# Kernel tuning notes

Hardware: AMD Instinct MI355X
Metric: run time of the kernel (lower is better)

## Reference

```python
import jax, jax.numpy as jnp
import numpy as np

B, P, Q, A, H = 8, 512, 64, 16, 128
H2, H10, G = 2 * H, 10 * H, 3 * H


def setup_inputs() -> dict:
    key = jax.random.key(0)
    ks = jax.random.split(key, 40)
    n = lambda k, s, sc=1.0: jax.random.normal(k, s, jnp.float32) * sc
    W = 0.05  # xavier-ish small init so tanh stays in linear-ish range
    inp = {
        "passage_enc": n(ks[0], (B, P, H2)),
        "query_enc": n(ks[1], (B, Q, H2)),
        "alt1_enc": n(ks[2], (B, A, H)),
        "alt2_enc": n(ks[3], (B, A, H)),
        "alt3_enc": n(ks[4], (B, A, H)),
        "a_att_w": n(ks[5], (H,), W),
        "Wc1": n(ks[6], (H2, H), W), "Wc2": n(ks[7], (H2, H), W), "vc": n(ks[8], (H,), W),
        "Wb": n(ks[9], (H2, H2), W),
        "Wd": n(ks[10], (H2, H), W), "vd": n(ks[11], (H,), W),
        "Wm": n(ks[12], (H2, H), W), "vm": n(ks[13], (H,), W),
        "wq": n(ks[14], (H2, H), W), "vq": n(ks[15], (H,), W),
        "wp1": n(ks[16], (H2, H), W), "wp2": n(ks[17], (H2, H), W), "vp": n(ks[18], (H,), W),
        "predict_w": n(ks[19], (H2, H), W),
        "gWih_f": n(ks[20], (H10, G), W), "gWhh_f": n(ks[21], (H, G), W),
        "gbih_f": jnp.zeros((G,), jnp.float32), "gbhh_f": jnp.zeros((G,), jnp.float32),
        "gWih_b": n(ks[22], (H10, G), W), "gWhh_b": n(ks[23], (H, G), W),
        "gbih_b": jnp.zeros((G,), jnp.float32), "gbhh_b": jnp.zeros((G,), jnp.float32),
        "passage_mask": jnp.ones((B, P), jnp.int32),
        "query_mask": jnp.ones((B, Q), jnp.int32),
        "alt1_mask": jnp.ones((B, A), jnp.int32),
        "alt2_mask": jnp.ones((B, A), jnp.int32),
        "alt3_mask": jnp.ones((B, A), jnp.int32),
    }
    return inp


def _att_pool(x, w, mask):
    # x: (B,T,D), w: (D,) -> (B,D) masked-softmax attention pooling
    s = jnp.where(mask != 0, x @ w, -jnp.inf)
    a = jax.nn.softmax(s, axis=1)
    return jnp.einsum('bt,btd->bd', a, x)


def _masked_attend(scores, qmask, query):
    # scores: (B,P,Q); mask over query axis, softmax over Q, weighted sum of query
    s = jnp.where(qmask[:, None, :] != 0, scores, -jnp.inf)
    a = jax.nn.softmax(s, axis=2)
    return jnp.einsum('bpq,bqd->bpd', a, query)


def _gru_dir(x, Wih, Whh, bih, bhh, reverse):
    # x: (B,T,Din) -> (B,T,H), PyTorch GRU gate convention
    if reverse:
        x = x[:, ::-1]
    gi = x @ Wih + bih  # (B,T,3H)
    h0 = jnp.zeros((x.shape[0], Whh.shape[0]), x.dtype)

    def step(h, gi_t):
        gh = h @ Whh + bhh
        i_r, i_z, i_n = jnp.split(gi_t, 3, axis=-1)
        h_r, h_z, h_n = jnp.split(gh, 3, axis=-1)
        r = jax.nn.sigmoid(i_r + h_r)
        z = jax.nn.sigmoid(i_z + h_z)
        nn_ = jnp.tanh(i_n + r * h_n)
        h_new = (1.0 - z) * nn_ + z * h
        return h_new, h_new

    _, ys = jax.lax.scan(step, h0, jnp.swapaxes(gi, 0, 1))
    ys = jnp.swapaxes(ys, 0, 1)
    if reverse:
        ys = ys[:, ::-1]
    return ys


def _forward(passage_enc, query_enc, alt1_enc, alt2_enc, alt3_enc,
             a_att_w, Wc1, Wc2, vc, Wb, Wd, vd, Wm, vm,
             wq, vq, wp1, wp2, vp, predict_w,
             gWih_f, gWhh_f, gbih_f, gbhh_f, gWih_b, gWhh_b, gbih_b, gbhh_b,
             passage_mask, query_mask, alt1_mask, alt2_mask, alt3_mask):
    # --- alternative-answer pooling ---
    a1 = _att_pool(alt1_enc, a_att_w, alt1_mask)
    a2 = _att_pool(alt2_enc, a_att_w, alt2_mask)
    a3 = _att_pool(alt3_enc, a_att_w, alt3_mask)

    # --- multi-hop passage-query attention (4 score variants) ---
    p1 = passage_enc @ Wc1          # (B,P,H)
    q1 = query_enc @ Wc2            # (B,Q,H)
    sc_c = jnp.einsum('bpqh,h->bpq', jnp.tanh(p1[:, :, None, :] + q1[:, None, :, :]), vc)
    pc = _masked_attend(sc_c, query_mask, query_enc)

    sc_b = jnp.einsum('bpd,bqd->bpq', passage_enc @ Wb, query_enc)
    pb = _masked_attend(sc_b, query_mask, query_enc)

    # Wd(p * q) with elementwise product, then tanh, then vd
    sc_d = jnp.einsum('bpqh,h->bpq',
                      jnp.tanh(jnp.einsum('bpk,bqk,kh->bpqh', passage_enc, query_enc, Wd)), vd)
    pd = _masked_attend(sc_d, query_mask, query_enc)

    # Wm(q - p) = q@Wm - p@Wm (linearity)
    pmq = query_enc @ Wm            # (B,Q,H)
    pmp = passage_enc @ Wm          # (B,P,H)
    sc_m = jnp.einsum('bpqh,h->bpq', jnp.tanh(pmq[:, None, :, :] - pmp[:, :, None, :]), vm)
    pm = _masked_attend(sc_m, query_mask, query_enc)

    # --- aggregation bi-GRU over (B,P,10H) ---
    agg_in = jnp.concatenate([passage_enc, pc, pb, pd, pm], axis=2)
    h_f = _gru_dir(agg_in, gWih_f, gWhh_f, gbih_f, gbhh_f, reverse=False)
    h_b = _gru_dir(agg_in, gWih_b, gWhh_b, gbih_b, gbhh_b, reverse=True)
    agg = jnp.concatenate([h_f, h_b], axis=2)   # (B,P,2H)

    # --- query summary rq ---
    sj = jnp.where(query_mask != 0, jnp.tanh(query_enc @ wq) @ vq, -jnp.inf)
    sj = jax.nn.softmax(sj, axis=1)
    rq = jnp.einsum('bq,bqd->bd', sj, query_enc)   # (B,2H)

    # --- passage summary rp attended by rq ---
    sp = jnp.tanh(agg @ wp1 + (rq @ wp2)[:, None, :]) @ vp   # (B,P)
    sp = jnp.where(passage_mask != 0, sp, -jnp.inf)
    sp = jax.nn.softmax(sp, axis=1)
    rp = jnp.einsum('bp,bpd->bd', sp, agg)          # (B,2H)
    rp = jax.nn.leaky_relu(rp @ predict_w)          # (B,H), slope 0.01

    alters = jnp.stack([a1, a2, a3], axis=1)        # (B,3,H)
    logits = jnp.einsum('bah,bh->ba', alters, rp)
    return jax.nn.softmax(logits, axis=1)


def reference(passage_enc, query_enc, alt1_enc, alt2_enc, alt3_enc,
              a_att_w, Wc1, Wc2, vc, Wb, Wd, vd, Wm, vm,
              wq, vq, wp1, wp2, vp, predict_w,
              gWih_f, gWhh_f, gbih_f, gbhh_f, gWih_b, gWhh_b, gbih_b, gbhh_b,
              passage_mask, query_mask, alt1_mask, alt2_mask, alt3_mask):
    return _forward(passage_enc, query_enc, alt1_enc, alt2_enc, alt3_enc,
                    a_att_w, Wc1, Wc2, vc, Wb, Wd, vd, Wm, vm,
                    wq, vq, wp1, wp2, vp, predict_w,
                    gWih_f, gWhh_f, gbih_f, gbhh_f, gWih_b, gWhh_b, gbih_b, gbhh_b,
                    passage_mask, query_mask, alt1_mask, alt2_mask, alt3_mask)
```

## Files before the change

### kernel.cpp

```cpp
#include <hip/hip_runtime.h>

#define B_ 8
#define P_ 512
#define Q_ 64
#define A_ 16
#define H_ 128
#define H2_ 256
#define H10_ 1280
#define G_ 384

typedef float f32x4 __attribute__((ext_vector_type(4)));
typedef _Float16 half4_t __attribute__((ext_vector_type(4)));
typedef _Float16 half8_t __attribute__((ext_vector_type(8)));

__device__ __forceinline__ float fast_tanh(float x) {
  return 1.f - 2.f * __builtin_amdgcn_rcpf(1.f + __builtin_amdgcn_exp2f(2.88539008f * x));
}
__device__ __forceinline__ float fast_sigm(float x) {
  return __builtin_amdgcn_rcpf(1.f + __builtin_amdgcn_exp2f(-1.44269504f * x));
}

#define GRUBAR() asm volatile("s_waitcnt lgkmcnt(0)\n\ts_barrier" ::: "memory")

#define NB_PRE 6936

__device__ __forceinline__ void prep_frag_body(int idx, const float* __restrict__ W,
                                               _Float16* __restrict__ out, int KT, int HT, int N) {
  int total = KT * HT * 64 * 4;
  if (idx >= total) return;
  int e = idx & 3;
  int l = (idx >> 2) & 63;
  int rest = idx >> 8;
  int ht = rest % HT;
  int ks = rest / HT;
  int k = ks * 16 + ((l >> 4) << 2) + e;
  int n = ht * 16 + (l & 15);
  out[idx] = (_Float16)W[(size_t)k * N + n];
}

__device__ __forceinline__ void prep_frag32_body(int idx, const float* __restrict__ W,
                                                 _Float16* __restrict__ out, int KT, int HT, int N) {
  int total = KT * HT * 64 * 8;
  if (idx >= total) return;
  int e = idx & 7;
  int l = (idx >> 3) & 63;
  int rest = idx >> 9;
  int ht = rest % HT;
  int ks = rest / HT;
  int k = ks * 32 + ((l >> 4) << 3) + e;
  int n = ht * 16 + (l & 15);
  out[idx] = (_Float16)W[(size_t)k * N + n];
}

__global__ __launch_bounds__(256) void k_pre(
    const float* __restrict__ a1, const float* __restrict__ a2, const float* __restrict__ a3,
    const int* __restrict__ m1, const int* __restrict__ m2, const int* __restrict__ m3,
    const float* __restrict__ a_att_w, float* __restrict__ alters,
    const float* __restrict__ Wd, _Float16* __restrict__ wd_sw,
    const float* __restrict__ gWih_f, const float* __restrict__ gWih_b,
    _Float16* __restrict__ gih_sw,
    const float* __restrict__ gWhh_f, const float* __restrict__ gWhh_b,
    _Float16* __restrict__ whh_sw,
    const float* __restrict__ pas, const float* __restrict__ qry,
    _Float16* __restrict__ pas_h,
    const float* __restrict__ Wc1, const float* __restrict__ Wm, const float* __restrict__ Wb,
    _Float16* __restrict__ wpc_sw,
    float* __restrict__ qryT,
    const float* __restrict__ Wc2, float* __restrict__ q1T, float* __restrict__ pmqT,
    const float* __restrict__ wq, const float* __restrict__ vq, float* __restrict__ sjraw) {
  int bx = blockIdx.x;
  int tid = threadIdx.x;
  if (bx < 24) {
    int b = bx / 3, i = bx % 3;
    const float* x = (i == 0) ? a1 : (i == 1) ? a2 : a3;
    const int* mk = (i == 0) ? m1 : (i == 1) ? m2 : m3;
    __shared__ float sc[A_];
    __shared__ float sw[A_];
    if (tid < A_) {
      const float* row = x + ((size_t)(b * A_ + tid)) * H_;
      float acc = 0.f;
      for (int h = 0; h < H_; ++h) acc += row[h] * a_att_w[h];
      sc[tid] = (mk[b * A_ + tid] != 0) ? acc : -1e30f;
    }
    __syncthreads();
    if (tid == 0) {
      float mx = -1e30f;
      for (int a = 0; a < A_; ++a) mx = fmaxf(mx, sc[a]);
      float s = 0.f;
      for (int a = 0; a < A_; ++a) { float e = __expf(sc[a] - mx); sw[a] = e; s += e; }
      float inv = 1.f / s;
      for (int a = 0; a < A_; ++a) sw[a] *= inv;
    }
    __syncthreads();
    if (tid < H_) {
      float acc = 0.f;
      for (int a = 0; a < A_; ++a) acc += sw[a] * x[((size_t)(b * A_ + a)) * H_ + tid];
      alters[((size_t)(b * 3 + i)) * H_ + tid] = acc;
    }
    return;
  }
  bx -= 24;
  if (bx < 128) { prep_frag_body(bx * 256 + tid, Wd, wd_sw, 16, 8, H_); return; }
  bx -= 128;
  if (bx < 1920) { prep_frag_body(bx * 256 + tid, gWih_f, gih_sw, 80, 24, G_); return; }
  bx -= 1920;
  if (bx < 1920) {
    prep_frag_body(bx * 256 + tid, gWih_b, gih_sw + (size_t)80 * 24 * 64 * 4, 80, 24, G_);
    return;
  }
  bx -= 1920;
  if (bx < 192) { prep_frag32_body(bx * 256 + tid, gWhh_f, whh_sw, 4, 24, G_); return; }
  bx -= 192;
  if (bx < 192) {
    prep_frag32_body(bx * 256 + tid, gWhh_b, whh_sw + (size_t)4 * 24 * 64 * 8, 4, 24, G_);
    return;
  }
  bx -= 192;
  if (bx < 1024) {
    int idx = bx * 256 + tid;
    float4 v = *(const float4*)(pas + (size_t)idx * 4);
    half4_t h;
    h[0] = (_Float16)v.x; h[1] = (_Float16)v.y; h[2] = (_Float16)v.z; h[3] = (_Float16)v.w;
    *(half4_t*)(pas_h + (size_t)idx * 4) = h;
    return;
  }
  bx -= 1024;
  if (bx < 512) {
    int idx = bx * 256 + tid;
    int e = idx & 3;
    int l = (idx >> 2) & 63;
    int rest = idx >> 8;
    int ht = rest & 31;
    int ks = rest >> 5;
    int k = ks * 16 + ((l >> 4) << 2) + e;
    int n = ht * 16 + (l & 15);
    float v = (n < 128) ? Wc1[(size_t)k * 128 + n]
            : (n < 256) ? Wm[(size_t)k * 128 + (n - 128)]
                        : Wb[(size_t)k * 256 + (n - 256)];
    wpc_sw[idx] = (_Float16)v;
    return;
  }
  bx -= 512;
  if (bx < 512) {
    int idx = bx * 256 + tid;
    int q = idx & 63;
    int d = (idx >> 6) & 255;
    int b = idx >> 14;
    qryT[idx] = qry[((size_t)(b * Q_ + q)) * H2_ + d];
    return;
  }
  bx -= 512;
  if (bx < 256) {
    int idx = bx * 256 + tid;
    int h = idx & 127;
    int rest = idx >> 7;
    int q = rest & 63;
    int b = rest >> 6;
    const float* qr = qry + ((size_t)(b * Q_ + q)) * H2_;
    float a1v = 0.f, a2v = 0.f;
#pragma unroll 4
    for (int d = 0; d < H2_; ++d) {
      float qv = qr[d];
      a1v += qv * Wc2[(size_t)d * H_ + h];
      a2v += qv * Wm[(size_t)d * H_ + h];
    }
    q1T[((size_t)(b * H_ + h)) * Q_ + q] = a1v;
    pmqT[((size_t)(b * H_ + h)) * Q_ + q] = a2v;
    return;
  }
  bx -= 256;
  {
    int rs = tid >> 7;
    int h = tid & 127;
    int row = bx * 2 + rs;
    const float* qr = qry + (size_t)row * H2_;
    float acc = 0.f;
#pragma unroll 4
    for (int d = 0; d < H2_; ++d) acc += qr[d] * wq[(size_t)d * H_ + h];
    float v = fast_tanh(acc) * vq[h];
    for (int m = 32; m >= 1; m >>= 1) v += __shfl_xor(v, m);
    __shared__ float par[2][2];
    if ((h & 63) == 0) par[rs][h >> 6] = v;
    __syncthreads();
    if (h == 0) sjraw[row] = par[rs][0] + par[rs][1];
  }
}

__global__ __launch_bounds__(256) void k_scd_rq(
    const float* __restrict__ pas, const float* __restrict__ qry,
    const _Float16* __restrict__ wd_sw, const float* __restrict__ vd,
    float* __restrict__ scd,
    const float* __restrict__ sjraw, const int* __restrict__ qmask,
    const float* __restrict__ wp2, float* __restrict__ rqw2,
    const _Float16* __restrict__ pas_h, const _Float16* __restrict__ wpc_sw,
    float* __restrict__ p1, float* __restrict__ pmp, float* __restrict__ pasWb) {
  int bx0 = blockIdx.x;
  int tid = threadIdx.x;
  if (bx0 < B_ * Q_ * 8) {
    int pt = bx0 & 7;
    int rem = bx0 >> 3;
    int q = rem & (Q_ - 1);
    int b = rem >> 6;
    int w = tid >> 6, l = tid & 63;
    __shared__ __align__(16) float qs[H2_];
    __shared__ float vds[H_];
    if (tid < H2_) qs[tid] = qry[((size_t)(b * Q_ + q)) * H2_ + tid];
    if (tid < H_) vds[tid] = vd[tid];
    __syncthreads();
    int arow = pt * 64 + w * 16 + (l & 15);
    const float* prow = pas + ((size_t)(b * P_) + arow) * H2_;
    int ko = (l >> 4) << 2;
    f32x4 acc[8] = {};
#pragma unroll
    for (int ks = 0; ks < 16; ++ks) {
      int j0 = ks * 16 + ko;
      float4 pa = *(const float4*)(prow + j0);
      float4 qa = *(const float4*)(qs + j0);
      half4_t a;
      a[0] = (_Float16)(pa.x * qa.x);
      a[1] = (_Float16)(pa.y * qa.y);
      a[2] = (_Float16)(pa.z * qa.z);
      a[3] = (_Float16)(pa.w * qa.w);
      const _Float16* bb = wd_sw + (((size_t)(ks * 8) * 64) + l) * 4;
#pragma unroll
      for (int ht = 0; ht < 8; ++ht) {
        half4_t bf = *(const half4_t*)(bb + (size_t)ht * 64 * 4);
        acc[ht] = __builtin_amdgcn_mfma_f32_16x16x16f16(a, bf, acc[ht], 0, 0, 0);
      }
    }
    float part[4] = {0.f, 0.f, 0.f, 0.f};
#pragma unroll
    for (int ht = 0; ht < 8; ++ht) {
      float v = vds[ht * 16 + (l & 15)];
#pragma unroll
      for (int j = 0; j < 4; ++j) part[j] += v * fast_tanh(acc[ht][j]);
    }
#pragma unroll
    for (int j = 0; j < 4; ++j) {
      float s = part[j];
      s += __shfl_xor(s, 1);
      s += __shfl_xor(s, 2);
      s += __shfl_xor(s, 4);
      s += __shfl_xor(s, 8);
      part[j] = s;
    }
    if ((l & 15) == 0) {
      int pr = pt * 64 + w * 16 + ((l >> 4) << 2);
#pragma unroll
      for (int j = 0; j < 4; ++j)
        scd[((size_t)b * P_ + pr + j) * Q_ + q] = part[j];
    }
    return;
  }
  if (bx0 < B_ * Q_ * 8 + B_) {
    int b = bx0 - B_ * Q_ * 8;
    int t = tid;
    __shared__ float sj[Q_];
    __shared__ float rql[H2_];
    if (t < Q_) {
      float s = (qmask[b * Q_ + t] != 0) ? sjraw[b * Q_ + t] : -1e30f;
      float mx = s;
      for (int m = 32; m >= 1; m >>= 1) mx = fmaxf(mx, __shfl_xor(mx, m));
      float e = __expf(s - mx);
      float sum = e;
      for (int m = 32; m >= 1; m >>= 1) sum += __shfl_xor(sum, m);
      sj[t] = e / sum;
    }
    __syncthreads();
    {
      float acc = 0.f;
      const float* qcol = qry + (size_t)b * Q_ * H2_ + t;
#pragma unroll 8
      for (int q = 0; q < Q_; ++q) acc += sj[q] * qcol[(size_t)q * H2_];
      rql[t] = acc;
    }
    __syncthreads();
    if (t < H_) {
      float acc = 0.f;
#pragma unroll 4
      for (int d = 0; d < H2_; ++d) acc += rql[d] * wp2[(size_t)d * H_ + t];
      rqw2[b * H_ + t] = acc;
    }
    return;
  }
  {
    int bx2 = bx0 - (B_ * Q_ * 8 + B_);
    int rt = bx2 >> 1, nh = bx2 & 1;
    int w = tid >> 6, l = tid & 63;
    int p0 = rt * 64 + w * 16;
    const _Float16* arow = pas_h + ((size_t)(p0 + (l & 15))) * H2_ + ((l >> 4) << 2);
    const _Float16* bbase = wpc_sw + (size_t)l * 4;
    f32x4 acc[16] = {};
    for (int ks = 0; ks < 16; ++ks) {
      half4_t a = *(const half4_t*)(arow + ks * 16);
      const _Float16* bkt = bbase + ((size_t)(ks * 32 + nh * 16)) * 64 * 4;
#pragma unroll
      for (int ht = 0; ht < 16; ++ht) {
        half4_t bf = *(const half4_t*)(bkt + (size_t)ht * 64 * 4);
        acc[ht] = __builtin_amdgcn_mfma_f32_16x16x16f16(a, bf, acc[ht], 0, 0, 0);
      }
    }
    int r0 = p0 + ((l >> 4) << 2);
#pragma unroll
    for (int ht = 0; ht < 16; ++ht) {
      int col = (nh * 16 + ht) * 16 + (l & 15);
#pragma unroll
      for (int j = 0; j < 4; ++j) {
        float v = acc[ht][j];
        size_t row = r0 + j;
        if (col < 128) p1[row * H_ + col] = v;
        else if (col < 256) pmp[row * H_ + (col - 128)] = v;
        else pasWb[row * H2_ + (col - 256)] = v;
      }
    }
  }
}

__global__ __launch_bounds__(256) void k_attend(
    const float* __restrict__ pas, const float* __restrict__ qry,
    const float* __restrict__ p1, const float* __restrict__ pmp,
    const float* __restrict__ q1T, const float* __restrict__ pmqT,
    const float* __restrict__ qryT,
    const float* __restrict__ pasWb, const float* __restrict__ scd,
    const float* __restrict__ vc, const float* __restrict__ vm,
    const int* __restrict__ qmask, _Float16* __restrict__ agg_h) {
  int bx = blockIdx.x;
  int b = bx >> 8, p0 = (bx & 255) * 2;
  int tid = threadIdx.x;
  __shared__ float p1s[2][H_], pmps[2][H_];
  __shared__ float pbs[2][H2_];
  __shared__ float sscd[2][Q_];
  __shared__ float ps[2][3][4][Q_];
  __shared__ float asw[2][4][Q_];
  size_t rowp = (size_t)b * P_ + p0;
  if (tid < 2 * H_) {
    int pp = tid >> 7, h = tid & 127;
    p1s[pp][h] = p1[(rowp + pp) * H_ + h];
    pmps[pp][h] = pmp[(rowp + pp) * H_ + h];
  }
  {
    int pp = tid >> 7, d2 = (tid & 127) * 2;
    pbs[pp][d2] = pasWb[(rowp + pp) * H2_ + d2];
    pbs[pp][d2 + 1] = pasWb[(rowp + pp) * H2_ + d2 + 1];
  }
  if (tid < 2 * Q_) sscd[tid >> 6][tid & 63] = scd[(rowp + (tid >> 6)) * Q_ + (tid & 63)];
  __syncthreads();
  {
    int q = tid & 63, part = tid >> 6;
    const float* q1b = q1T + (size_t)b * H_ * Q_;
    const float* pmqb = pmqT + (size_t)b * H_ * Q_;
    const float* qTb = qryT + (size_t)b * H2_ * Q_;
    float sc0 = 0.f, sc1 = 0.f, sm0 = 0.f, sm1 = 0.f, sb0 = 0.f, sb1 = 0.f;
    int h0 = part * 32;
#pragma unroll 4
    for (int i = 0; i < 32; ++i) {
      int h = h0 + i;
      float q1v = q1b[h * Q_ + q];
      float pmqv = pmqb[h * Q_ + q];
      float vcv = vc[h], vmv = vm[h];
      sc0 += fast_tanh(p1s[0][h] + q1v) * vcv;
      sc1 += fast_tanh(p1s[1][h] + q1v) * vcv;
      sm0 += fast_tanh(pmqv - pmps[0][h]) * vmv;
      sm1 += fast_tanh(pmqv - pmps[1][h]) * vmv;
    }
    int d0 = part * 64;
#pragma unroll 4
    for (int i = 0; i < 64; ++i) {
      int d = d0 + i;
      float qv = qTb[d * Q_ + q];
      sb0 += pbs[0][d] * qv;
      sb1 += pbs[1][d] * qv;
    }
    ps[0][0][part][q] = sc0;
    ps[1][0][part][q] = sc1;
    ps[0][1][part][q] = sb0;
    ps[1][1][part][q] = sb1;
    ps[0][2][part][q] = sm0;
    ps[1][2][part][q] = sm1;
  }
  __syncthreads();
  {
    int wv = tid >> 6, lane = tid & 63;
    int msk = (qmask[b * Q_ + lane] != 0);
#pragma unroll
    for (int pp = 0; pp < 2; ++pp) {
      float s;
      if (wv == 2) s = sscd[pp][lane];
      else {
        int arr = (wv == 3) ? 2 : wv;
        s = (ps[pp][arr][0][lane] + ps[pp][arr][1][lane]) +
            (ps[pp][arr][2][lane] + ps[pp][arr][3][lane]);
      }
      s = msk ? s : -1e30f;
      float mx = s;
      for (int m = 32; m >= 1; m >>= 1) mx = fmaxf(mx, __shfl_xor(mx, m));
      float e = __expf(s - mx);
      float sum = e;
      for (int m = 32; m >= 1; m >>= 1) sum += __shfl_xor(sum, m);
      asw[pp][wv][lane] = e / sum;
    }
  }
  __syncthreads();
  {
    int d = tid;
    const float* qcol = qry + (size_t)b * Q_ * H2_ + d;
    float o00 = 0.f, o01 = 0.f, o02 = 0.f, o03 = 0.f;
    float o10 = 0.f, o11 = 0.f, o12 = 0.f, o13 = 0.f;
#pragma unroll 8
    for (int q2 = 0; q2 < Q_; ++q2) {
      float qv = qcol[(size_t)q2 * H2_];
      o00 += asw[0][0][q2] * qv;
      o01 += asw[0][1][q2] * qv;
      o02 += asw[0][2][q2] * qv;
      o03 += asw[0][3][q2] * qv;
      o10 += asw[1][0][q2] * qv;
      o11 += asw[1][1][q2] * qv;
      o12 += asw[1][2][q2] * qv;
      o13 += asw[1][3][q2] * qv;
    }
    _Float16* arow0 = agg_h + rowp * H10_;
    arow0[d] = (_Float16)pas[rowp * H2_ + d];
    arow0[256 + d] = (_Float16)o00;
    arow0[512 + d] = (_Float16)o01;
    arow0[768 + d] = (_Float16)o02;
    arow0[1024 + d] = (_Float16)o03;
    _Float16* arow1 = agg_h + (rowp + 1) * H10_;
    arow1[d] = (_Float16)pas[(rowp + 1) * H2_ + d];
    arow1[256 + d] = (_Float16)o10;
    arow1[512 + d] = (_Float16)o11;
    arow1[768 + d] = (_Float16)o12;
    arow1[1024 + d] = (_Float16)o13;
  }
}

__global__ __launch_bounds__(256) void k_gi(
    const _Float16* __restrict__ agg_h, const _Float16* __restrict__ gih_sw,
    const float* __restrict__ gbih_f, const float* __restrict__ gbih_b,
    float* __restrict__ gi_f, float* __restrict__ gi_b) {
  int dir = blockIdx.y;
  const float* gbih = dir ? gbih_b : gbih_f;
  float* gi = dir ? gi_b : gi_f;
  int tid = threadIdx.x;
  int w = tid >> 6, l = tid & 63;
  int p0 = blockIdx.x * 64 + w * 16;
  const _Float16* arow = agg_h + ((size_t)(p0 + (l & 15))) * H10_ + ((l >> 4) << 2);
  const _Float16* bbase = gih_sw + (size_t)dir * 80 * 24 * 64 * 4 + (size_t)l * 4;
  f32x4 acc[24] = {};
  for (int ks = 0; ks < 80; ++ks) {
    half4_t a = *(const half4_t*)(arow + ks * 16);
    const _Float16* bkt = bbase + (size_t)ks * 24 * 64 * 4;
#pragma unroll
    for (int ht = 0; ht < 24; ++ht) {
      half4_t bf = *(const half4_t*)(bkt + (size_t)ht * 64 * 4);
      acc[ht] = __builtin_amdgcn_mfma_f32_16x16x16f16(a, bf, acc[ht], 0, 0, 0);
    }
  }
  int r0 = p0 + ((l >> 4) << 2);
#pragma unroll
  for (int ht = 0; ht < 24; ++ht) {
    int col = ht * 16 + (l & 15);
    float bias = gbih[col];
#pragma unroll
    for (int j = 0; j < 4; ++j)
      gi[((size_t)(r0 + j)) * G_ + col] = acc[ht][j] + bias;
  }
}

__global__ __attribute__((amdgpu_waves_per_eu(1, 1))) __launch_bounds__(256) void k_gru(
    const float* __restrict__ gi_f, const float* __restrict__ gi_b,
    const _Float16* __restrict__ whh_sw,
    const float* __restrict__ bhh_f, const float* __restrict__ bhh_b,
    float* __restrict__ agg) {
  int dir = blockIdx.x >> 3;
  int bb = blockIdx.x & 7;
  const float* gi = dir ? gi_b : gi_f;
  const float* bhh = dir ? bhh_b : bhh_f;
  int tid = threadIdx.x;
  int w = tid >> 6, l = tid & 63;
  int j0 = w * 32 + (l & 15);
  int j1 = j0 + 16;
  half8_t Bf[3][2][4];
  {
    const _Float16* wb = whh_sw + (size_t)dir * 4 * 24 * 64 * 8;
#pragma unroll
    for (int g = 0; g < 3; ++g)
#pragma unroll
      for (int cc = 0; cc < 2; ++cc) {
        int ct = g * 8 + w * 2 + cc;
#pragma unroll
        for (int ks = 0; ks < 4; ++ks)
          Bf[g][cc][ks] = *(const half8_t*)(wb + (((size_t)(ks * 24 + ct)) * 64 + l) * 8);
      }
  }
  float bhr0 = bhh[j0], bhz0 = bhh[128 + j0], bhn0 = bhh[256 + j0];
  float bhr1 = bhh[j1], bhz1 = bhh[128 + j1], bhn1 = bhh[256 + j1];
  __shared__ __align__(16) _Float16 hsbuf[2][H_];
  if (tid < H_) hsbuf[0][tid] = (_Float16)0.f;
  float hprev0 = 0.f, hprev1 = 0.f;
  int p = dir ? (P_ - 1) : 0;
  int dp = dir ? -1 : 1;
  size_t gbase = (size_t)bb * P_;
  float g0[6], g1[6];
  {
    size_t r0 = (gbase + p) * G_;
    g0[0] = gi[r0 + j0]; g0[1] = gi[r0 + 128 + j0]; g0[2] = gi[r0 + 256 + j0];
    g0[3] = gi[r0 + j1]; g0[4] = gi[r0 + 128 + j1]; g0[5] = gi[r0 + 256 + j1];
    size_t r1 = (gbase + p + dp) * G_;
    g1[0] = gi[r1 + j0]; g1[1] = gi[r1 + 128 + j0]; g1[2] = gi[r1 + 256 + j0];
    g1[3] = gi[r1 + j1]; g1[4] = gi[r1 + 128 + j1]; g1[5] = gi[r1 + 256 + j1];
  }
  GRUBAR();
  int cur = 0;
  int ao = (l >> 4) << 3;
  for (int t = 0; t < P_; ++t) {
    float g2[6] = {};
    if (t + 2 < P_) {
      size_t r2 = (gbase + p + 2 * dp) * G_;
      g2[0] = gi[r2 + j0]; g2[1] = gi[r2 + 128 + j0]; g2[2] = gi[r2 + 256 + j0];
      g2[3] = gi[r2 + j1]; g2[4] = gi[r2 + 128 + j1]; g2[5] = gi[r2 + 256 + j1];
    }
    const _Float16* hb = hsbuf[cur];
    half8_t ha[4];
#pragma unroll
    for (int ks = 0; ks < 4; ++ks) ha[ks] = *(const half8_t*)(hb + ks * 32 + ao);
    f32x4 ar0 = {}, ar1 = {}, az0 = {}, az1 = {}, an0 = {}, an1 = {};
#pragma unroll
    for (int ks = 0; ks < 4; ++ks) {
      ar0 = __builtin_amdgcn_mfma_f32_16x16x32_f16(ha[ks], Bf[0][0][ks], ar0, 0, 0, 0);
      az0 = __builtin_amdgcn_mfma_f32_16x16x32_f16(ha[ks], Bf[1][0][ks], az0, 0, 0, 0);
      an0 = __builtin_amdgcn_mfma_f32_16x16x32_f16(ha[ks], Bf[2][0][ks], an0, 0, 0, 0);
      ar1 = __builtin_amdgcn_mfma_f32_16x16x32_f16(ha[ks], Bf[0][1][ks], ar1, 0, 0, 0);
      az1 = __builtin_amdgcn_mfma_f32_16x16x32_f16(ha[ks], Bf[1][1][ks], az1, 0, 0, 0);
      an1 = __builtin_amdgcn_mfma_f32_16x16x32_f16(ha[ks], Bf[2][1][ks], an1, 0, 0, 0);
    }
    float r0v = fast_sigm(g0[0] + ar0[0] + bhr0);
    float z0v = fast_sigm(g0[1] + az0[0] + bhz0);
    float n0v = fast_tanh(g0[2] + r0v * (an0[0] + bhn0));
    float h0v = (1.f - z0v) * n0v + z0v * hprev0;
    float r1v = fast_sigm(g0[3] + ar1[0] + bhr1);
    float z1v = fast_sigm(g0[4] + az1[0] + bhz1);
    float n1v = fast_tanh(g0[5] + r1v * (an1[0] + bhn1));
    float h1v = (1.f - z1v) * n1v + z1v * hprev1;
    hprev0 = h0v;
    hprev1 = h1v;
    if (l < 16) {
      hsbuf[cur ^ 1][j0] = (_Float16)h0v;
      hsbuf[cur ^ 1][j1] = (_Float16)h1v;
      float* arow = agg + (size_t)(gbase + p) * H2_ + dir * H_;
      arow[j0] = h0v;
      arow[j1] = h1v;
    }
    GRUBAR();
    cur ^= 1;
#pragma unroll
    for (int i = 0; i < 6; ++i) { g0[i] = g1[i]; g1[i] = g2[i]; }
    p += dp;
  }
}

__global__ __launch_bounds__(128) void k_spscore(
    const float* __restrict__ agg, const float* __restrict__ wp1,
    const float* __restrict__ rqw2, const float* __restrict__ vp,
    float* __restrict__ spraw) {
  int bx = blockIdx.x;
  int b = bx >> 6, p0 = (bx & 63) * 8;
  int h = threadIdx.x;
  const float* ar = agg + ((size_t)b * P_ + p0) * H2_;
  float base = rqw2[b * H_ + h];
  float acc[8];
#pragma unroll
  for (int r = 0; r < 8; ++r) acc[r] = base;
#pragma unroll 4
  for (int d = 0; d < H2_; ++d) {
    float wv = wp1[(size_t)d * H_ + h];
#pragma unroll
    for (int r = 0; r < 8; ++r) acc[r] += ar[(size_t)r * H2_ + d] * wv;
  }
  __shared__ float par[8][2];
  float vph = vp[h];
#pragma unroll
  for (int r = 0; r < 8; ++r) {
    float v = fast_tanh(acc[r]) * vph;
    for (int m = 32; m >= 1; m >>= 1) v += __shfl_xor(v, m);
    if ((h & 63) == 0) par[r][h >> 6] = v;
  }
  __syncthreads();
  if (h < 8) spraw[(size_t)b * P_ + p0 + h] = par[h][0] + par[h][1];
}

__global__ __launch_bounds__(256) void k_final(
    const float* __restrict__ spraw, const int* __restrict__ pmask,
    const float* __restrict__ agg, const float* __restrict__ predict_w,
    const float* __restrict__ alters, float* __restrict__ out) {
  int b = blockIdx.x;
  int t = threadIdx.x;
  __shared__ float sp[P_];
  __shared__ float red[4];
  __shared__ float rpr[H2_];
  __shared__ float rpl[H_];
  __shared__ float lg[3];
  float s0 = (pmask[b * P_ + t] != 0) ? spraw[b * P_ + t] : -1e30f;
  float s1 = (pmask[b * P_ + 256 + t] != 0) ? spraw[b * P_ + 256 + t] : -1e30f;
  float mx = fmaxf(s0, s1);
  for (int m = 32; m >= 1; m >>= 1) mx = fmaxf(mx, __shfl_xor(mx, m));
  if ((t & 63) == 0) red[t >> 6] = mx;
  __syncthreads();
  mx = fmaxf(fmaxf(red[0], red[1]), fmaxf(red[2], red[3]));
  float e0 = __expf(s0 - mx), e1 = __expf(s1 - mx);
  float ss = e0 + e1;
  for (int m = 32; m >= 1; m >>= 1) ss += __shfl_xor(ss, m);
  __syncthreads();
  if ((t & 63) == 0) red[t >> 6] = ss;
  __syncthreads();
  float tot = red[0] + red[1] + red[2] + red[3];
  float inv = 1.f / tot;
  sp[t] = e0 * inv;
  sp[256 + t] = e1 * inv;
  __syncthreads();
  {
    float acc = 0.f;
    const float* acol = agg + (size_t)b * P_ * H2_ + t;
#pragma unroll 8
    for (int p = 0; p < P_; ++p) acc += sp[p] * acol[(size_t)p * H2_];
    rpr[t] = acc;
  }
  __syncthreads();
  if (t < H_) {
    float acc = 0.f;
#pragma unroll 4
    for (int d = 0; d < H2_; ++d) acc += rpr[d] * predict_w[(size_t)d * H_ + t];
    rpl[t] = (acc > 0.f) ? acc : 0.01f * acc;
  }
  __syncthreads();
  if (t < 3) {
    float acc = 0.f;
    const float* al = alters + ((size_t)(b * 3 + t)) * H_;
    for (int h = 0; h < H_; ++h) acc += al[h] * rpl[h];
    lg[t] = acc;
  }
  __syncthreads();
  if (t == 0) {
    float m3 = fmaxf(lg[0], fmaxf(lg[1], lg[2]));
    float x0 = __expf(lg[0] - m3), x1 = __expf(lg[1] - m3), x2 = __expf(lg[2] - m3);
    float is = 1.f / (x0 + x1 + x2);
    out[b * 3 + 0] = x0 * is;
    out[b * 3 + 1] = x1 * is;
    out[b * 3 + 2] = x2 * is;
  }
}

extern "C" void kernel_launch(void* const* d_in, const int* in_sizes, int n_in,
                              void* d_out, int out_size, void* d_ws, size_t ws_size,
                              hipStream_t stream) {
  (void)in_sizes; (void)n_in; (void)out_size; (void)ws_size;
  const float* pas = (const float*)d_in[0];
  const float* qry = (const float*)d_in[1];
  const float* alt1 = (const float*)d_in[2];
  const float* alt2 = (const float*)d_in[3];
  const float* alt3 = (const float*)d_in[4];
  const float* a_att_w = (const float*)d_in[5];
  const float* Wc1 = (const float*)d_in[6];
  const float* Wc2 = (const float*)d_in[7];
  const float* vc = (const float*)d_in[8];
  const float* Wb = (const float*)d_in[9];
  const float* Wd = (const float*)d_in[10];
  const float* vd = (const float*)d_in[11];
  const float* Wm = (const float*)d_in[12];
  const float* vm = (const float*)d_in[13];
  const float* wq = (const float*)d_in[14];
  const float* vq = (const float*)d_in[15];
  const float* wp1 = (const float*)d_in[16];
  const float* wp2 = (const float*)d_in[17];
  const float* vp = (const float*)d_in[18];
  const float* predict_w = (const float*)d_in[19];
  const float* gWih_f = (const float*)d_in[20];
  const float* gWhh_f = (const float*)d_in[21];
  const float* gbih_f = (const float*)d_in[22];
  const float* gbhh_f = (const float*)d_in[23];
  const float* gWih_b = (const float*)d_in[24];
  const float* gWhh_b = (const float*)d_in[25];
  const float* gbih_b = (const float*)d_in[26];
  const float* gbhh_b = (const float*)d_in[27];
  const int* pmask = (const int*)d_in[28];
  const int* qmask = (const int*)d_in[29];
  const int* m1 = (const int*)d_in[30];
  const int* m2 = (const int*)d_in[31];
  const int* m3 = (const int*)d_in[32];
  float* out = (float*)d_out;

  char* ws = (char*)d_ws;
  size_t off = 0;
  auto alloc_f = [&](size_t n) {
    float* ptr = (float*)(ws + off);
    off += n * 4;
    off = (off + 255) & ~(size_t)255;
    return ptr;
  };
  float* alters = alloc_f((size_t)B_ * 3 * H_);
  float* p1 = alloc_f((size_t)B_ * P_ * H_);
  float* pmp = alloc_f((size_t)B_ * P_ * H_);
  float* pasWb = alloc_f((size_t)B_ * P_ * H2_);
  float* scd = alloc_f((size_t)B_ * P_ * Q_);
  float* gi_f = alloc_f((size_t)B_ * P_ * G_);
  float* gi_b = alloc_f((size_t)B_ * P_ * G_);
  float* agg = alloc_f((size_t)B_ * P_ * H2_);
  float* sjraw = alloc_f((size_t)B_ * Q_);
  float* rqw2 = alloc_f((size_t)B_ * H_);
  float* spraw = alloc_f((size_t)B_ * P_);
  float* q1T = alloc_f((size_t)B_ * H_ * Q_);
  float* pmqT = alloc_f((size_t)B_ * H_ * Q_);
  float* qryT = alloc_f((size_t)B_ * H2_ * Q_);
  auto alloc_h = [&](size_t n) {
    _Float16* ptr = (_Float16*)(ws + off);
    off += n * 2;
    off = (off + 255) & ~(size_t)255;
    return ptr;
  };
  _Float16* wd_sw = alloc_h((size_t)16 * 8 * 64 * 4);
  _Float16* gih_sw = alloc_h((size_t)2 * 80 * 24 * 64 * 4);
  _Float16* agg_h = alloc_h((size_t)B_ * P_ * H10_);
  _Float16* whh_sw = alloc_h((size_t)2 * 4 * 24 * 64 * 8);
  _Float16* pas_h = alloc_h((size_t)B_ * P_ * H2_);
  _Float16* wpc_sw = alloc_h((size_t)16 * 32 * 64 * 4);

  k_pre<<<NB_PRE, 256, 0, stream>>>(
      alt1, alt2, alt3, m1, m2, m3, a_att_w, alters,
      Wd, wd_sw, gWih_f, gWih_b, gih_sw, gWhh_f, gWhh_b, whh_sw,
      pas, qry, pas_h, Wc1, Wm, Wb, wpc_sw, qryT, Wc2, q1T, pmqT, wq, vq, sjraw);
  k_scd_rq<<<B_ * Q_ * 8 + B_ + 128, 256, 0, stream>>>(
      pas, qry, wd_sw, vd, scd, sjraw, qmask, wp2, rqw2,
      pas_h, wpc_sw, p1, pmp, pasWb);
  k_attend<<<B_ * P_ / 2, 256, 0, stream>>>(
      pas, qry, p1, pmp, q1T, pmqT, qryT, pasWb, scd, vc, vm, qmask, agg_h);
  k_gi<<<dim3(64, 2), 256, 0, stream>>>(agg_h, gih_sw, gbih_f, gbih_b, gi_f, gi_b);
  k_gru<<<16, 256, 0, stream>>>(gi_f, gi_b, whh_sw, gbhh_f, gbhh_b, agg);
  k_spscore<<<B_ * P_ / 8, 128, 0, stream>>>(agg, wp1, rqw2, vp, spraw);
  k_final<<<B_, 256, 0, stream>>>(spraw, pmask, agg, predict_w, alters, out);
}
```

Measured before the change: 661.5 us.

## Vectorize prep packing, batch scd over 8 queries, widen GRU to 512 threads

The weight-fragment prep paths now pack 4 or 8 fp16 values per thread, so k_pre needs far fewer blocks and issues wide stores. k_scd_rq stages Wd fragments in LDS and reuses fp16 passage rows across 8 queries per block, which cuts repeated global reads of the fp32 passage. The GRU recurrence spreads over 8 waves with one hidden unit per lane and two independent MFMA accumulator chains, shortening the serial per-step MFMA chain at the cost of a wider barrier. Multiplying the passage by the query from fp16 storage changes rounding slightly.

Result: faster. 549.6 us (-16.9%).

```diff
diff --git a/kernel.cpp b/kernel.cpp
--- a/kernel.cpp
+++ b/kernel.cpp
@@ -22,34 +22,38 @@
 
 #define GRUBAR() asm volatile("s_waitcnt lgkmcnt(0)\n\ts_barrier" ::: "memory")
 
-#define NB_PRE 6936
-
-__device__ __forceinline__ void prep_frag_body(int idx, const float* __restrict__ W,
-                                               _Float16* __restrict__ out, int KT, int HT, int N) {
-  int total = KT * HT * 64 * 4;
+#define NB_PRE 2344
+
+__device__ __forceinline__ void prep_frag4_body(int idx, const float* __restrict__ W,
+                                                _Float16* __restrict__ out, int KT, int HT, int N) {
+  int total = KT * HT * 64;
   if (idx >= total) return;
-  int e = idx & 3;
-  int l = (idx >> 2) & 63;
-  int rest = idx >> 8;
+  int l = idx & 63;
+  int rest = idx >> 6;
   int ht = rest % HT;
   int ks = rest / HT;
-  int k = ks * 16 + ((l >> 4) << 2) + e;
+  int k = ks * 16 + ((l >> 4) << 2);
   int n = ht * 16 + (l & 15);
-  out[idx] = (_Float16)W[(size_t)k * N + n];
-}
-
-__device__ __forceinline__ void prep_frag32_body(int idx, const float* __restrict__ W,
-                                                 _Float16* __restrict__ out, int KT, int HT, int N) {
-  int total = KT * HT * 64 * 8;
+  half4_t o;
+#pragma unroll
+  for (int e = 0; e < 4; ++e) o[e] = (_Float16)W[(size_t)(k + e) * N + n];
+  *(half4_t*)(out + (size_t)idx * 4) = o;
+}
+
+__device__ __forceinline__ void prep_frag32_8_body(int idx, const float* __restrict__ W,
+                                                   _Float16* __restrict__ out, int KT, int HT, int N) {
+  int total = KT * HT * 64;
   if (idx >= total) return;
-  int e = idx & 7;
-  int l = (idx >> 3) & 63;
-  int rest = idx >> 9;
+  int l = idx & 63;
+  int rest = idx >> 6;
   int ht = rest % HT;
   int ks = rest / HT;
-  int k = ks * 32 + ((l >> 4) << 3) + e;
+  int k = ks * 32 + ((l >> 4) << 3);
   int n = ht * 16 + (l & 15);
-  out[idx] = (_Float16)W[(size_t)k * N + n];
+  half8_t o;
+#pragma unroll
+  for (int e = 0; e < 8; ++e) o[e] = (_Float16)W[(size_t)(k + e) * N + n];
+  *(half8_t*)(out + (size_t)idx * 8) = o;
 }
 
 __global__ __launch_bounds__(256) void k_pre(
@@ -100,56 +104,68 @@
     return;
   }
   bx -= 24;
-  if (bx < 128) { prep_frag_body(bx * 256 + tid, Wd, wd_sw, 16, 8, H_); return; }
-  bx -= 128;
-  if (bx < 1920) { prep_frag_body(bx * 256 + tid, gWih_f, gih_sw, 80, 24, G_); return; }
-  bx -= 1920;
-  if (bx < 1920) {
-    prep_frag_body(bx * 256 + tid, gWih_b, gih_sw + (size_t)80 * 24 * 64 * 4, 80, 24, G_);
-    return;
-  }
-  bx -= 1920;
-  if (bx < 192) { prep_frag32_body(bx * 256 + tid, gWhh_f, whh_sw, 4, 24, G_); return; }
-  bx -= 192;
-  if (bx < 192) {
-    prep_frag32_body(bx * 256 + tid, gWhh_b, whh_sw + (size_t)4 * 24 * 64 * 8, 4, 24, G_);
-    return;
-  }
-  bx -= 192;
-  if (bx < 1024) {
-    int idx = bx * 256 + tid;
-    float4 v = *(const float4*)(pas + (size_t)idx * 4);
-    half4_t h;
-    h[0] = (_Float16)v.x; h[1] = (_Float16)v.y; h[2] = (_Float16)v.z; h[3] = (_Float16)v.w;
-    *(half4_t*)(pas_h + (size_t)idx * 4) = h;
-    return;
-  }
-  bx -= 1024;
+  if (bx < 32) { prep_frag4_body(bx * 256 + tid, Wd, wd_sw, 16, 8, H_); return; }
+  bx -= 32;
+  if (bx < 480) { prep_frag4_body(bx * 256 + tid, gWih_f, gih_sw, 80, 24, G_); return; }
+  bx -= 480;
+  if (bx < 480) {
+    prep_frag4_body(bx * 256 + tid, gWih_b, gih_sw + (size_t)80 * 24 * 64 * 4, 80, 24, G_);
+    return;
+  }
+  bx -= 480;
+  if (bx < 24) { prep_frag32_8_body(bx * 256 + tid, gWhh_f, whh_sw, 4, 24, G_); return; }
+  bx -= 24;
+  if (bx < 24) {
+    prep_frag32_8_body(bx * 256 + tid, gWhh_b, whh_sw + (size_t)4 * 24 * 64 * 8, 4, 24, G_);
+    return;
+  }
+  bx -= 24;
   if (bx < 512) {
     int idx = bx * 256 + tid;
-    int e = idx & 3;
-    int l = (idx >> 2) & 63;
-    int rest = idx >> 8;
+    float4 v0 = *(const float4*)(pas + (size_t)idx * 8);
+    float4 v1 = *(const float4*)(pas + (size_t)idx * 8 + 4);
+    half8_t h;
+    h[0] = (_Float16)v0.x; h[1] = (_Float16)v0.y; h[2] = (_Float16)v0.z; h[3] = (_Float16)v0.w;
+    h[4] = (_Float16)v1.x; h[5] = (_Float16)v1.y; h[6] = (_Float16)v1.z; h[7] = (_Float16)v1.w;
+    *(half8_t*)(pas_h + (size_t)idx * 8) = h;
+    return;
+  }
+  bx -= 512;
+  if (bx < 128) {
+    int idx = bx * 256 + tid;
+    int l = idx & 63;
+    int rest = idx >> 6;
     int ht = rest & 31;
     int ks = rest >> 5;
-    int k = ks * 16 + ((l >> 4) << 2) + e;
+    int k = ks * 16 + ((l >> 4) << 2);
     int n = ht * 16 + (l & 15);
-    float v = (n < 128) ? Wc1[(size_t)k * 128 + n]
-            : (n < 256) ? Wm[(size_t)k * 128 + (n - 128)]
-                        : Wb[(size_t)k * 256 + (n - 256)];
-    wpc_sw[idx] = (_Float16)v;
-    return;
-  }
-  bx -= 512;
-  if (bx < 512) {
+    half4_t o;
+#pragma unroll
+    for (int e = 0; e < 4; ++e) {
+      int kk = k + e;
+      float v = (n < 128) ? Wc1[(size_t)kk * 128 + n]
+              : (n < 256) ? Wm[(size_t)kk * 128 + (n - 128)]
+                          : Wb[(size_t)kk * 256 + (n - 256)];
+      o[e] = (_Float16)v;
+    }
+    *(half4_t*)(wpc_sw + (size_t)idx * 4) = o;
+    return;
+  }
+  bx -= 128;
+  if (bx < 128) {
     int idx = bx * 256 + tid;
-    int q = idx & 63;
-    int d = (idx >> 6) & 255;
-    int b = idx >> 14;
-    qryT[idx] = qry[((size_t)(b * Q_ + q)) * H2_ + d];
-    return;
-  }
-  bx -= 512;
+    int q4 = idx & 15;
+    int d = (idx >> 4) & 255;
+    int b = idx >> 12;
+    float4 o;
+    o.x = qry[((size_t)(b * Q_ + q4 * 4 + 0)) * H2_ + d];
+    o.y = qry[((size_t)(b * Q_ + q4 * 4 + 1)) * H2_ + d];
+    o.z = qry[((size_t)(b * Q_ + q4 * 4 + 2)) * H2_ + d];
+    o.w = qry[((size_t)(b * Q_ + q4 * 4 + 3)) * H2_ + d];
+    *(float4*)(qryT + ((size_t)(b * H2_ + d)) * Q_ + q4 * 4) = o;
+    return;
+  }
+  bx -= 128;
   if (bx < 256) {
     int idx = bx * 256 + tid;
     int h = idx & 127;
@@ -187,76 +203,88 @@
 }
 
 __global__ __launch_bounds__(256) void k_scd_rq(
-    const float* __restrict__ pas, const float* __restrict__ qry,
+    const float* __restrict__ qry,
     const _Float16* __restrict__ wd_sw, const float* __restrict__ vd,
     float* __restrict__ scd,
     const float* __restrict__ sjraw, const int* __restrict__ qmask,
     const float* __restrict__ wp2, float* __restrict__ rqw2,
     const _Float16* __restrict__ pas_h, const _Float16* __restrict__ wpc_sw,
     float* __restrict__ p1, float* __restrict__ pmp, float* __restrict__ pasWb) {
+  __shared__ __align__(16) char smem[65536 + 8192 + 512];
   int bx0 = blockIdx.x;
   int tid = threadIdx.x;
-  if (bx0 < B_ * Q_ * 8) {
-    int pt = bx0 & 7;
-    int rem = bx0 >> 3;
-    int q = rem & (Q_ - 1);
-    int b = rem >> 6;
-    int w = tid >> 6, l = tid & 63;
-    __shared__ __align__(16) float qs[H2_];
-    __shared__ float vds[H_];
-    if (tid < H2_) qs[tid] = qry[((size_t)(b * Q_ + q)) * H2_ + tid];
+  if (bx0 < 512) {
+    int b = bx0 >> 6;
+    int pt = (bx0 >> 3) & 7;
+    int qg = bx0 & 7;
+    _Float16* wlds = (_Float16*)smem;
+    float (*qs8)[H2_] = (float(*)[H2_])(smem + 65536);
+    float* vds = (float*)(smem + 65536 + 8192);
+    {
+      const uint4* wsrc = (const uint4*)wd_sw;
+      uint4* wdst = (uint4*)wlds;
+#pragma unroll
+      for (int i = 0; i < 16; ++i) wdst[tid + 256 * i] = wsrc[tid + 256 * i];
+    }
+#pragma unroll
+    for (int qi = 0; qi < 8; ++qi)
+      qs8[qi][tid] = qry[((size_t)(b * Q_ + qg * 8 + qi)) * H2_ + tid];
     if (tid < H_) vds[tid] = vd[tid];
     __syncthreads();
-    int arow = pt * 64 + w * 16 + (l & 15);
-    const float* prow = pas + ((size_t)(b * P_) + arow) * H2_;
+    int w = tid >> 6, l = tid & 63;
     int ko = (l >> 4) << 2;
-    f32x4 acc[8] = {};
-#pragma unroll
-    for (int ks = 0; ks < 16; ++ks) {
-      int j0 = ks * 16 + ko;
-      float4 pa = *(const float4*)(prow + j0);
-      float4 qa = *(const float4*)(qs + j0);
-      half4_t a;
-      a[0] = (_Float16)(pa.x * qa.x);
-      a[1] = (_Float16)(pa.y * qa.y);
-      a[2] = (_Float16)(pa.z * qa.z);
-      a[3] = (_Float16)(pa.w * qa.w);
-      const _Float16* bb = wd_sw + (((size_t)(ks * 8) * 64) + l) * 4;
+    const _Float16* prow = pas_h + ((size_t)(b * P_) + pt * 64 + w * 16 + (l & 15)) * H2_ + ko;
+    half4_t pah[16];
+#pragma unroll
+    for (int ks = 0; ks < 16; ++ks) pah[ks] = *(const half4_t*)(prow + ks * 16);
+    for (int qi = 0; qi < 8; ++qi) {
+      f32x4 acc[8] = {};
+#pragma unroll
+      for (int ks = 0; ks < 16; ++ks) {
+        float4 qa = *(const float4*)(&qs8[qi][ks * 16 + ko]);
+        half4_t a;
+        a[0] = (_Float16)((float)pah[ks][0] * qa.x);
+        a[1] = (_Float16)((float)pah[ks][1] * qa.y);
+        a[2] = (_Float16)((float)pah[ks][2] * qa.z);
+        a[3] = (_Float16)((float)pah[ks][3] * qa.w);
+        const _Float16* bb = wlds + (((size_t)(ks * 8)) * 64 + l) * 4;
+#pragma unroll
+        for (int ht = 0; ht < 8; ++ht) {
+          half4_t bf = *(const half4_t*)(bb + (size_t)ht * 64 * 4);
+          acc[ht] = __builtin_amdgcn_mfma_f32_16x16x16f16(a, bf, acc[ht], 0, 0, 0);
+        }
+      }
+      float part[4] = {0.f, 0.f, 0.f, 0.f};
 #pragma unroll
       for (int ht = 0; ht < 8; ++ht) {
-        half4_t bf = *(const half4_t*)(bb + (size_t)ht * 64 * 4);
-        acc[ht] = __builtin_amdgcn_mfma_f32_16x16x16f16(a, bf, acc[ht], 0, 0, 0);
+        float v = vds[ht * 16 + (l & 15)];
+#pragma unroll
+        for (int j = 0; j < 4; ++j) part[j] += v * fast_tanh(acc[ht][j]);
       }
-    }
-    float part[4] = {0.f, 0.f, 0.f, 0.f};
-#pragma unroll
-    for (int ht = 0; ht < 8; ++ht) {
-      float v = vds[ht * 16 + (l & 15)];
-#pragma unroll
-      for (int j = 0; j < 4; ++j) part[j] += v * fast_tanh(acc[ht][j]);
-    }
-#pragma unroll
-    for (int j = 0; j < 4; ++j) {
-      float s = part[j];
-      s += __shfl_xor(s, 1);
-      s += __shfl_xor(s, 2);
-      s += __shfl_xor(s, 4);
-      s += __shfl_xor(s, 8);
-      part[j] = s;
-    }
-    if ((l & 15) == 0) {
-      int pr = pt * 64 + w * 16 + ((l >> 4) << 2);
-#pragma unroll
-      for (int j = 0; j < 4; ++j)
-        scd[((size_t)b * P_ + pr + j) * Q_ + q] = part[j];
-    }
-    return;
-  }
-  if (bx0 < B_ * Q_ * 8 + B_) {
-    int b = bx0 - B_ * Q_ * 8;
+#pragma unroll
+      for (int j = 0; j < 4; ++j) {
+        float s = part[j];
+        s += __shfl_xor(s, 1);
+        s += __shfl_xor(s, 2);
+        s += __shfl_xor(s, 4);
+        s += __shfl_xor(s, 8);
+        part[j] = s;
+      }
+      if ((l & 15) == 0) {
+        int pr = pt * 64 + w * 16 + ((l >> 4) << 2);
+        int q = qg * 8 + qi;
+#pragma unroll
+        for (int j = 0; j < 4; ++j)
+          scd[((size_t)b * P_ + pr + j) * Q_ + q] = part[j];
+      }
+    }
+    return;
+  }
+  if (bx0 < 512 + B_) {
+    int b = bx0 - 512;
     int t = tid;
-    __shared__ float sj[Q_];
-    __shared__ float rql[H2_];
+    float* sj = (float*)smem;
+    float* rql = (float*)(smem + Q_ * 4);
     if (t < Q_) {
       float s = (qmask[b * Q_ + t] != 0) ? sjraw[b * Q_ + t] : -1e30f;
       float mx = s;
@@ -284,7 +312,7 @@
     return;
   }
   {
-    int bx2 = bx0 - (B_ * Q_ * 8 + B_);
+    int bx2 = bx0 - (512 + B_);
     int rt = bx2 >> 1, nh = bx2 & 1;
     int w = tid >> 6, l = tid & 63;
     int p0 = rt * 64 + w * 16;
@@ -466,7 +494,7 @@
   }
 }
 
-__global__ __attribute__((amdgpu_waves_per_eu(1, 1))) __launch_bounds__(256) void k_gru(
+__global__ __attribute__((amdgpu_waves_per_eu(2, 2))) __launch_bounds__(512) void k_gru(
     const float* __restrict__ gi_f, const float* __restrict__ gi_b,
     const _Float16* __restrict__ whh_sw,
     const float* __restrict__ bhh_f, const float* __restrict__ bhh_b,
@@ -477,83 +505,74 @@
   const float* bhh = dir ? bhh_b : bhh_f;
   int tid = threadIdx.x;
   int w = tid >> 6, l = tid & 63;
-  int j0 = w * 32 + (l & 15);
-  int j1 = j0 + 16;
-  half8_t Bf[3][2][4];
+  int j = w * 16 + (l & 15);
+  half8_t Bf[3][4];
   {
     const _Float16* wb = whh_sw + (size_t)dir * 4 * 24 * 64 * 8;
 #pragma unroll
-    for (int g = 0; g < 3; ++g)
-#pragma unroll
-      for (int cc = 0; cc < 2; ++cc) {
-        int ct = g * 8 + w * 2 + cc;
-#pragma unroll
-        for (int ks = 0; ks < 4; ++ks)
-          Bf[g][cc][ks] = *(const half8_t*)(wb + (((size_t)(ks * 24 + ct)) * 64 + l) * 8);
-      }
-  }
-  float bhr0 = bhh[j0], bhz0 = bhh[128 + j0], bhn0 = bhh[256 + j0];
-  float bhr1 = bhh[j1], bhz1 = bhh[128 + j1], bhn1 = bhh[256 + j1];
+    for (int g = 0; g < 3; ++g) {
+      int ct = g * 8 + w;
+#pragma unroll
+      for (int ks = 0; ks < 4; ++ks)
+        Bf[g][ks] = *(const half8_t*)(wb + (((size_t)(ks * 24 + ct)) * 64 + l) * 8);
+    }
+  }
+  float bhr = bhh[j], bhz = bhh[128 + j], bhn = bhh[256 + j];
   __shared__ __align__(16) _Float16 hsbuf[2][H_];
   if (tid < H_) hsbuf[0][tid] = (_Float16)0.f;
-  float hprev0 = 0.f, hprev1 = 0.f;
+  float hprev = 0.f;
   int p = dir ? (P_ - 1) : 0;
   int dp = dir ? -1 : 1;
   size_t gbase = (size_t)bb * P_;
-  float g0[6], g1[6];
+  float g0r, g0z, g0n, g1r, g1z, g1n;
   {
     size_t r0 = (gbase + p) * G_;
-    g0[0] = gi[r0 + j0]; g0[1] = gi[r0 + 128 + j0]; g0[2] = gi[r0 + 256 + j0];
-    g0[3] = gi[r0 + j1]; g0[4] = gi[r0 + 128 + j1]; g0[5] = gi[r0 + 256 + j1];
+    g0r = gi[r0 + j]; g0z = gi[r0 + 128 + j]; g0n = gi[r0 + 256 + j];
     size_t r1 = (gbase + p + dp) * G_;
-    g1[0] = gi[r1 + j0]; g1[1] = gi[r1 + 128 + j0]; g1[2] = gi[r1 + 256 + j0];
-    g1[3] = gi[r1 + j1]; g1[4] = gi[r1 + 128 + j1]; g1[5] = gi[r1 + 256 + j1];
+    g1r = gi[r1 + j]; g1z = gi[r1 + 128 + j]; g1n = gi[r1 + 256 + j];
   }
   GRUBAR();
   int cur = 0;
   int ao = (l >> 4) << 3;
   for (int t = 0; t < P_; ++t) {
-    float g2[6] = {};
+    float g2r = 0.f, g2z = 0.f, g2n = 0.f;
     if (t + 2 < P_) {
       size_t r2 = (gbase + p + 2 * dp) * G_;
-      g2[0] = gi[r2 + j0]; g2[1] = gi[r2 + 128 + j0]; g2[2] = gi[r2 + 256 + j0];
-      g2[3] = gi[r2 + j1]; g2[4] = gi[r2 + 128 + j1]; g2[5] = gi[r2 + 256 + j1];
+      g2r = gi[r2 + j]; g2z = gi[r2 + 128 + j]; g2n = gi[r2 + 256 + j];
     }
     const _Float16* hb = hsbuf[cur];
     half8_t ha[4];
 #pragma unroll
     for (int ks = 0; ks < 4; ++ks) ha[ks] = *(const half8_t*)(hb + ks * 32 + ao);
-    f32x4 ar0 = {}, ar1 = {}, az0 = {}, az1 = {}, an0 = {}, an1 = {};
-#pragma unroll
-    for (int ks = 0; ks < 4; ++ks) {
-      ar0 = __builtin_amdgcn_mfma_f32_16x16x32_f16(ha[ks], Bf[0][0][ks], ar0, 0, 0, 0);
-      az0 = __builtin_amdgcn_mfma_f32_16x16x32_f16(ha[ks], Bf[1][0][ks], az0, 0, 0, 0);
-      an0 = __builtin_amdgcn_mfma_f32_16x16x32_f16(ha[ks], Bf[2][0][ks], an0, 0, 0, 0);
-      ar1 = __builtin_amdgcn_mfma_f32_16x16x32_f16(ha[ks], Bf[0][1][ks], ar1, 0, 0, 0);
-      az1 = __builtin_amdgcn_mfma_f32_16x16x32_f16(ha[ks], Bf[1][1][ks], az1, 0, 0, 0);
-      an1 = __builtin_amdgcn_mfma_f32_16x16x32_f16(ha[ks], Bf[2][1][ks], an1, 0, 0, 0);
-    }
-    float r0v = fast_sigm(g0[0] + ar0[0] + bhr0);
-    float z0v = fast_sigm(g0[1] + az0[0] + bhz0);
-    float n0v = fast_tanh(g0[2] + r0v * (an0[0] + bhn0));
-    float h0v = (1.f - z0v) * n0v + z0v * hprev0;
-    float r1v = fast_sigm(g0[3] + ar1[0] + bhr1);
-    float z1v = fast_sigm(g0[4] + az1[0] + bhz1);
-    float n1v = fast_tanh(g0[5] + r1v * (an1[0] + bhn1));
-    float h1v = (1.f - z1v) * n1v + z1v * hprev1;
-    hprev0 = h0v;
-    hprev1 = h1v;
+    f32x4 arL = {}, arH = {}, azL = {}, azH = {}, anL = {}, anH = {};
+    arL = __builtin_amdgcn_mfma_f32_16x16x32_f16(ha[0], Bf[0][0], arL, 0, 0, 0);
+    azL = __builtin_amdgcn_mfma_f32_16x16x32_f16(ha[0], Bf[1][0], azL, 0, 0, 0);
+    anL = __builtin_amdgcn_mfma_f32_16x16x32_f16(ha[0], Bf[2][0], anL, 0, 0, 0);
+    arH = __builtin_amdgcn_mfma_f32_16x16x32_f16(ha[2], Bf[0][2], arH, 0, 0, 0);
+    azH = __builtin_amdgcn_mfma_f32_16x16x32_f16(ha[2], Bf[1][2], azH, 0, 0, 0);
+    anH = __builtin_amdgcn_mfma_f32_16x16x32_f16(ha[2], Bf[2][2], anH, 0, 0, 0);
+    arL = __builtin_amdgcn_mfma_f32_16x16x32_f16(ha[1], Bf[0][1], arL, 0, 0, 0);
+    azL = __builtin_amdgcn_mfma_f32_16x16x32_f16(ha[1], Bf[1][1], azL, 0, 0, 0);
+    anL = __builtin_amdgcn_mfma_f32_16x16x32_f16(ha[1], Bf[2][1], anL, 0, 0, 0);
+    arH = __builtin_amdgcn_mfma_f32_16x16x32_f16(ha[3], Bf[0][3], arH, 0, 0, 0);
+    azH = __builtin_amdgcn_mfma_f32_16x16x32_f16(ha[3], Bf[1][3], azH, 0, 0, 0);
+    anH = __builtin_amdgcn_mfma_f32_16x16x32_f16(ha[3], Bf[2][3], anH, 0, 0, 0);
+    float arS = arL[0] + arH[0];
+    float azS = azL[0] + azH[0];
+    float anS = anL[0] + anH[0];
+    float r = fast_sigm(g0r + arS + bhr);
+    float z = fast_sigm(g0z + azS + bhz);
+    float nn = fast_tanh(g0n + r * (anS + bhn));
+    float hnew = (1.f - z) * nn + z * hprev;
+    hprev = hnew;
     if (l < 16) {
-      hsbuf[cur ^ 1][j0] = (_Float16)h0v;
-      hsbuf[cur ^ 1][j1] = (_Float16)h1v;
-      float* arow = agg + (size_t)(gbase + p) * H2_ + dir * H_;
-      arow[j0] = h0v;
-      arow[j1] = h1v;
+      hsbuf[cur ^ 1][j] = (_Float16)hnew;
+      agg[(size_t)(gbase + p) * H2_ + dir * H_ + j] = hnew;
     }
     GRUBAR();
     cur ^= 1;
-#pragma unroll
-    for (int i = 0; i < 6; ++i) { g0[i] = g1[i]; g1[i] = g2[i]; }
+    g0r = g1r; g0z = g1z; g0n = g1n;
+    g1r = g2r; g1z = g2z; g1n = g2n;
     p += dp;
   }
 }
@@ -727,13 +746,13 @@
       alt1, alt2, alt3, m1, m2, m3, a_att_w, alters,
       Wd, wd_sw, gWih_f, gWih_b, gih_sw, gWhh_f, gWhh_b, whh_sw,
       pas, qry, pas_h, Wc1, Wm, Wb, wpc_sw, qryT, Wc2, q1T, pmqT, wq, vq, sjraw);
-  k_scd_rq<<<B_ * Q_ * 8 + B_ + 128, 256, 0, stream>>>(
-      pas, qry, wd_sw, vd, scd, sjraw, qmask, wp2, rqw2,
+  k_scd_rq<<<512 + B_ + 128, 256, 0, stream>>>(
+      qry, wd_sw, vd, scd, sjraw, qmask, wp2, rqw2,
       pas_h, wpc_sw, p1, pmp, pasWb);
   k_attend<<<B_ * P_ / 2, 256, 0, stream>>>(
       pas, qry, p1, pmp, q1T, pmqT, qryT, pasWb, scd, vc, vm, qmask, agg_h);
   k_gi<<<dim3(64, 2), 256, 0, stream>>>(agg_h, gih_sw, gbih_f, gbih_b, gi_f, gi_b);
-  k_gru<<<16, 256, 0, stream>>>(gi_f, gi_b, whh_sw, gbhh_f, gbhh_b, agg);
+  k_gru<<<16, 512, 0, stream>>>(gi_f, gi_b, whh_sw, gbhh_f, gbhh_b, agg);
   k_spscore<<<B_ * P_ / 8, 128, 0, stream>>>(agg, wp1, rqw2, vp, spraw);
   k_final<<<B_, 256, 0, stream>>>(spraw, pmask, agg, predict_w, alters, out);
 }
```
